# Kernel optimization log

Hardware: AMD Instinct MI355X
Metric: run time of the kernel (lower is better)

The kernel has to match this reference:

```python
import jax, jax.numpy as jnp
import numpy as np

D = 32       # d_model / hidden_size
H = 4        # n_heads
E = D // H   # head dim = 8
N = 2000     # nodes (hardcoded in FourierBlock weights / proj_class)
L = 96       # seq_len
MODES = (1, 4, 5)  # self.index hardcoded in FourierBlock
KAVG = 25    # moving_avg kernel (first of kernel list; layer uses res[0], trends[0])


def setup_inputs() -> dict:
    key = jax.random.key(0)
    ks = jax.random.split(key, 12)
    B = 8
    x = jax.random.normal(ks[0], (B, N, L, D), jnp.float32)
    lin = lambda k: jax.random.normal(k, (D, D), jnp.float32) * (1.0 / np.sqrt(D))
    scale = 1.0 / (D * D)  # FourierBlock: scale * torch.rand(...)
    W1 = jax.random.uniform(ks[5], (N, H, E, E, len(MODES)), jnp.float32) * scale
    W2 = jax.random.uniform(ks[6], (N, H, E, E, len(MODES)), jnp.float32) * scale
    return {
        "x": x,
        "Wq": lin(ks[1]), "bq": jnp.zeros((D,), jnp.float32),
        "Wk": lin(ks[2]), "bk": jnp.zeros((D,), jnp.float32),
        "Wv": lin(ks[3]), "bv": jnp.zeros((D,), jnp.float32),
        "Wo": lin(ks[4]), "bo": jnp.zeros((D,), jnp.float32),
        "W1": W1, "W2": W2,
    }


def _fourier_block(q, W1, W2):
    # q: [B, N, L, H, E] -> permute to [B, N, H, E, L] (torch: x = q.permute(0,1,3,4,2))
    B, Nn, Ll, Hh, Ee = q.shape
    xq = jnp.transpose(q, (0, 1, 3, 4, 2))
    x_ft = jnp.fft.rfft(xq, axis=-1)                 # [B, N, H, E, L//2+1] complex
    idx = jnp.array(MODES)
    xm = x_ft[..., idx]                              # [B, N, H, E, M]
    Wc = W1 + 1j * W2                                # complex per-node frequency weights
    out_m = jnp.einsum('bnhem,nheom->bnhom', xm, Wc.astype(jnp.complex64))
    F = Ll // 2 + 1
    out_ft = jnp.zeros((B, Nn, Hh, Ee, F), jnp.complex64).at[..., idx].set(out_m)
    y = jnp.fft.irfft(out_ft, n=Ll, axis=-1)         # [B, N, H, E, L]
    return jnp.transpose(y, (0, 1, 4, 2, 3))         # [B, N, L, H, E]


def _moving_avg(x, k):
    # replicate-pad the time axis by (k-1)//2 on each side, then mean over window k (stride 1)
    pad = (k - 1) // 2
    xp = jnp.pad(x, ((0, 0), (0, 0), (pad, pad), (0, 0)), mode='edge')
    cs = jnp.cumsum(xp, axis=2)
    cs = jnp.concatenate([jnp.zeros_like(cs[:, :, :1]), cs], axis=2)
    return (cs[:, :, k:] - cs[:, :, :-k]) / k        # [B, N, T, C]


def reference(x, Wq, bq, Wk, bk, Wv, bv, Wo, bo, W1, W2):
    B, Nn, Ll, Dm = x.shape
    # AutoCorrelationLayer projections
    q = (x @ Wq.T + bq).reshape(B, Nn, Ll, H, E)
    k = (x @ Wk.T + bk).reshape(B, Nn, Ll, H, E)   # faithful: computed, unused by FourierBlock
    v = (x @ Wv.T + bv).reshape(B, Nn, Ll, H, E)   # faithful: computed, unused by FourierBlock
    out = _fourier_block(q, W1, W2)                 # inner_correlation(q, k, v)
    out = out.reshape(B, Nn, Ll, Dm)
    new_x = out @ Wo.T + bo                         # out_projection
    # FFTDecompLayer: residual + series decomposition (eval mode, dropout=0)
    xr = x + new_x
    trend = _moving_avg(xr, KAVG)
    res = xr - trend
    return res
```

## Files before the change

kernel.cpp:

```cpp
#include <hip/hip_runtime.h>


#define N_NODES 2000

__global__ __launch_bounds__(256, 4)
void fused_fourier_decomp(const float* __restrict__ x,
                          const float* __restrict__ Wq,
                          const float* __restrict__ Wo,
                          const float* __restrict__ bo,
                          const float* __restrict__ W1,
                          const float* __restrict__ W2,
                          float* __restrict__ out)
{
  __shared__ __align__(16) float xT[32 * 97];
  __shared__ __align__(16) float basis[96 * 8];
  __shared__ __align__(16) float Wq_s[32 * 33];
  __shared__ __align__(16) float Wo_s[32 * 33];
  __shared__ __align__(16) float W1_s[768];
  __shared__ __align__(16) float W2_s[768];
  __shared__ __align__(16) float CS[32 * 8];
  __shared__ __align__(16) float X_s[32 * 8];
  __shared__ __align__(16) float O_s[32 * 8];
  __shared__ __align__(16) float Z_s[32 * 8];
  __shared__ float bo_s[32];
  float* const pp = xT;

  const int t = threadIdx.x;
  const int bid = blockIdx.x;
  const int n = bid % N_NODES;
  const size_t base = (size_t)bid * (96 * 32);

  const int d = t & 31;
  const int g = t >> 5;
  const int l0 = g * 12;

  float xv[12];
#pragma unroll
  for (int i = 0; i < 12; ++i)
    xv[i] = x[base + (size_t)(l0 + i) * 32 + d];

  for (int i = t; i < 1024; i += 256) {
    Wq_s[(i >> 5) * 33 + (i & 31)] = Wq[i];
    Wo_s[(i >> 5) * 33 + (i & 31)] = Wo[i];
  }
  {
    const float* W1p = W1 + n * 768;
    const float* W2p = W2 + n * 768;
    for (int i = t; i < 768; i += 256) {
      W1_s[i] = W1p[i];
      W2_s[i] = W2p[i];
    }
  }
  if (t < 32) bo_s[t] = bo[t];

  if (t < 96) {
    const int modes[3] = {1, 4, 5};
#pragma unroll
    for (int m = 0; m < 3; ++m) {
      int r = (modes[m] * t) % 96;
      float ang = (float)r * (6.28318530717958647692f / 96.0f);
      float sv, cv;
      sincosf(ang, &sv, &cv);
      basis[t * 8 + m] = cv;
      basis[t * 8 + 3 + m] = sv;
    }
    basis[t * 8 + 6] = 0.0f;
    basis[t * 8 + 7] = 0.0f;
  }
  __syncthreads();

  {
    float a0 = 0.f, a1 = 0.f, a2 = 0.f, a3 = 0.f, a4 = 0.f, a5 = 0.f;
#pragma unroll
    for (int i = 0; i < 12; ++i) {
      const int l = l0 + i;
      const float4 b0 = *(const float4*)&basis[l * 8];
      const float2 b1 = *(const float2*)&basis[l * 8 + 4];
      const float v = xv[i];
      a0 = fmaf(v, b0.x, a0);
      a1 = fmaf(v, b0.y, a1);
      a2 = fmaf(v, b0.z, a2);
      a3 = fmaf(v, b0.w, a3);
      a4 = fmaf(v, b1.x, a4);
      a5 = fmaf(v, b1.y, a5);
    }
    pp[g * 192 + 0 * 32 + d] = a0;
    pp[g * 192 + 1 * 32 + d] = a1;
    pp[g * 192 + 2 * 32 + d] = a2;
    pp[g * 192 + 3 * 32 + d] = a3;
    pp[g * 192 + 4 * 32 + d] = a4;
    pp[g * 192 + 5 * 32 + d] = a5;
  }
  __syncthreads();
  if (t < 192) {
    const int dd = t & 31, j = t >> 5;
    float s = 0.f;
#pragma unroll
    for (int gg = 0; gg < 8; ++gg) s += pp[gg * 192 + j * 32 + dd];
    CS[dd * 8 + j] = s;
  }
  __syncthreads();

  {
    float a0 = 0.f, a1 = 0.f, a2 = 0.f, a3 = 0.f, a4 = 0.f, a5 = 0.f;
#pragma unroll
    for (int i = 0; i < 4; ++i) {
      const int dd = g * 4 + i;
      const float w = Wq_s[d * 33 + dd];
      const float4 b0 = *(const float4*)&CS[dd * 8];
      const float2 b1 = *(const float2*)&CS[dd * 8 + 4];
      a0 = fmaf(w, b0.x, a0);
      a1 = fmaf(w, b0.y, a1);
      a2 = fmaf(w, b0.z, a2);
      a3 = fmaf(w, b0.w, a3);
      a4 = fmaf(w, b1.x, a4);
      a5 = fmaf(w, b1.y, a5);
    }
    pp[g * 192 + 0 * 32 + d] = a0;
    pp[g * 192 + 1 * 32 + d] = a1;
    pp[g * 192 + 2 * 32 + d] = a2;
    pp[g * 192 + 3 * 32 + d] = a3;
    pp[g * 192 + 4 * 32 + d] = a4;
    pp[g * 192 + 5 * 32 + d] = a5;
  }
  __syncthreads();
  if (t < 192) {
    const int c = t & 31, j = t >> 5;
    float s = 0.f;
#pragma unroll
    for (int gg = 0; gg < 8; ++gg) s += pp[gg * 192 + j * 32 + c];
    X_s[c * 8 + j] = (j < 3) ? s : -s;
  }
  __syncthreads();

  if (t < 96) {
    const int h = t / 24;
    const int r = t % 24;
    const int o = r / 3;
    const int m = r % 3;
    float re = 0.f, im = 0.f;
#pragma unroll
    for (int e = 0; e < 8; ++e) {
      const int c = h * 8 + e;
      const float xre = X_s[c * 8 + m];
      const float xim = X_s[c * 8 + 3 + m];
      const int wi = (c * 8 + o) * 3 + m;
      const float w1 = W1_s[wi], w2 = W2_s[wi];
      re = fmaf(xre, w1, re);
      re = fmaf(-xim, w2, re);
      im = fmaf(xre, w2, im);
      im = fmaf(xim, w1, im);
    }
    const int cp = h * 8 + o;
    O_s[cp * 8 + m] = re;
    O_s[cp * 8 + 3 + m] = im;
  }
  __syncthreads();

  {
    float a0 = 0.f, a1 = 0.f, a2 = 0.f, a3 = 0.f, a4 = 0.f, a5 = 0.f;
#pragma unroll
    for (int i = 0; i < 4; ++i) {
      const int c = g * 4 + i;
      const float w = Wo_s[d * 33 + c];
      const float4 b0 = *(const float4*)&O_s[c * 8];
      const float2 b1 = *(const float2*)&O_s[c * 8 + 4];
      a0 = fmaf(w, b0.x, a0);
      a1 = fmaf(w, b0.y, a1);
      a2 = fmaf(w, b0.z, a2);
      a3 = fmaf(w, b0.w, a3);
      a4 = fmaf(w, b1.x, a4);
      a5 = fmaf(w, b1.y, a5);
    }
    pp[g * 192 + 0 * 32 + d] = a0;
    pp[g * 192 + 1 * 32 + d] = a1;
    pp[g * 192 + 2 * 32 + d] = a2;
    pp[g * 192 + 3 * 32 + d] = a3;
    pp[g * 192 + 4 * 32 + d] = a4;
    pp[g * 192 + 5 * 32 + d] = a5;
  }
  __syncthreads();
  if (t < 192) {
    const int c = t & 31, j = t >> 5;
    float s = 0.f;
#pragma unroll
    for (int gg = 0; gg < 8; ++gg) s += pp[gg * 192 + j * 32 + c];
    Z_s[c * 8 + j] = s;
  }
  __syncthreads();

  float xr[12];
  {
    const float4 z0 = *(const float4*)&Z_s[d * 8];
    const float2 z1 = *(const float2*)&Z_s[d * 8 + 4];
    const float bov = bo_s[d];
#pragma unroll
    for (int i = 0; i < 12; ++i) {
      const int l = l0 + i;
      const float4 b0 = *(const float4*)&basis[l * 8];
      const float2 b1 = *(const float2*)&basis[l * 8 + 4];
      const float v = z0.x * b0.x + z0.y * b0.y + z0.z * b0.z
                    - z0.w * b0.w - z1.x * b1.x - z1.y * b1.y;
      const float r = fmaf(v, (1.0f / 48.0f), bov) + xv[i];
      xr[i] = r;
      xT[d * 97 + l] = r;
    }
  }
  __syncthreads();

  {
    const float* col = &xT[d * 97];
    float lowv[12];
    float S = 0.f;
#pragma unroll
    for (int j = 0; j < 12; ++j) {
      int idx = l0 - 12 + j;
      idx = idx < 0 ? 0 : idx;
      lowv[j] = col[idx];
      S += lowv[j];
    }
#pragma unroll
    for (int i = 0; i < 12; ++i) S += xr[i];
    {
      int idx = l0 + 12;
      idx = idx > 95 ? 95 : idx;
      S += col[idx];
    }
#pragma unroll
    for (int i = 0; i < 12; ++i) {
      const int l = l0 + i;
      const float res = xr[i] - S * (1.0f / 25.0f);
      out[base + (size_t)l * 32 + d] = res;
      int hi = l + 13;
      hi = hi > 95 ? 95 : hi;
      S += col[hi] - lowv[i];
    }
  }
}

extern "C" void kernel_launch(void* const* d_in, const int* in_sizes, int n_in,
                              void* d_out, int out_size, void* d_ws, size_t ws_size,
                              hipStream_t stream) {
  (void)n_in; (void)out_size; (void)d_ws; (void)ws_size;
  const float* x  = (const float*)d_in[0];
  const float* Wq = (const float*)d_in[1];
  const float* Wo = (const float*)d_in[7];
  const float* bo = (const float*)d_in[8];
  const float* W1 = (const float*)d_in[9];
  const float* W2 = (const float*)d_in[10];
  float* out = (float*)d_out;

  const int blocks = in_sizes[0] / (96 * 32);
  fused_fourier_decomp<<<blocks, 256, 0, stream>>>(x, Wq, Wo, bo, W1, W2, out);
}
```

Measured before the change: 386.2 us.

## Shrink shared memory, read weights from global, and raise occupancy target

Drops the per-block shared-memory staging of Wq, Wo, W1 and W2 and has the projection and mode-mixing stages read weights straight from global/L2. The Wq and Wo projections are restructured as a single 192-thread dot-product pass each, which removes one partial-sum stage and its barrier per projection. All scratch buffers are packed into one shared array with stride-9 padding, and the launch bounds request 8 blocks per CU. The aim is less shared memory and fewer barriers per block so more blocks fit per CU. The cost is redundant global weight reads and less thread-level parallelism in the projections.

```diff
diff --git a/kernel.cpp b/kernel.cpp
--- a/kernel.cpp
+++ b/kernel.cpp
@@ -3,7 +3,7 @@
 
 #define N_NODES 2000
 
-__global__ __launch_bounds__(256, 4)
+__global__ __launch_bounds__(256, 8)
 void fused_fourier_decomp(const float* __restrict__ x,
                           const float* __restrict__ Wq,
                           const float* __restrict__ Wo,
@@ -12,18 +12,15 @@
                           const float* __restrict__ W2,
                           float* __restrict__ out)
 {
-  __shared__ __align__(16) float xT[32 * 97];
-  __shared__ __align__(16) float basis[96 * 8];
-  __shared__ __align__(16) float Wq_s[32 * 33];
-  __shared__ __align__(16) float Wo_s[32 * 33];
-  __shared__ __align__(16) float W1_s[768];
-  __shared__ __align__(16) float W2_s[768];
-  __shared__ __align__(16) float CS[32 * 8];
-  __shared__ __align__(16) float X_s[32 * 8];
-  __shared__ __align__(16) float O_s[32 * 8];
-  __shared__ __align__(16) float Z_s[32 * 8];
-  __shared__ float bo_s[32];
-  float* const pp = xT;
+  __shared__ __align__(16) float smem[5056];
+  float* const basis = smem;
+  float* const CS    = smem + 768;
+  float* const Xs    = smem + 1056;
+  float* const Os    = smem + 1344;
+  float* const Zs    = smem + 1632;
+  float* const bos   = smem + 1920;
+  float* const xT    = smem + 1952;
+  float* const pp    = smem + 1952;
 
   const int t = threadIdx.x;
   const int bid = blockIdx.x;
@@ -34,24 +31,12 @@
   const int g = t >> 5;
   const int l0 = g * 12;
 
+  const float* xp = x + base + (size_t)l0 * 32 + d;
   float xv[12];
 #pragma unroll
-  for (int i = 0; i < 12; ++i)
-    xv[i] = x[base + (size_t)(l0 + i) * 32 + d];
-
-  for (int i = t; i < 1024; i += 256) {
-    Wq_s[(i >> 5) * 33 + (i & 31)] = Wq[i];
-    Wo_s[(i >> 5) * 33 + (i & 31)] = Wo[i];
-  }
-  {
-    const float* W1p = W1 + n * 768;
-    const float* W2p = W2 + n * 768;
-    for (int i = t; i < 768; i += 256) {
-      W1_s[i] = W1p[i];
-      W2_s[i] = W2p[i];
-    }
-  }
-  if (t < 32) bo_s[t] = bo[t];
+  for (int i = 0; i < 12; ++i) xv[i] = xp[i * 32];
+
+  if (t < 32) bos[t] = bo[t];
 
   if (t < 96) {
     const int modes[3] = {1, 4, 5};
@@ -97,110 +82,82 @@
     float s = 0.f;
 #pragma unroll
     for (int gg = 0; gg < 8; ++gg) s += pp[gg * 192 + j * 32 + dd];
-    CS[dd * 8 + j] = s;
-  }
-  __syncthreads();
-
-  {
-    float a0 = 0.f, a1 = 0.f, a2 = 0.f, a3 = 0.f, a4 = 0.f, a5 = 0.f;
-#pragma unroll
-    for (int i = 0; i < 4; ++i) {
-      const int dd = g * 4 + i;
-      const float w = Wq_s[d * 33 + dd];
-      const float4 b0 = *(const float4*)&CS[dd * 8];
-      const float2 b1 = *(const float2*)&CS[dd * 8 + 4];
-      a0 = fmaf(w, b0.x, a0);
-      a1 = fmaf(w, b0.y, a1);
-      a2 = fmaf(w, b0.z, a2);
-      a3 = fmaf(w, b0.w, a3);
-      a4 = fmaf(w, b1.x, a4);
-      a5 = fmaf(w, b1.y, a5);
-    }
-    pp[g * 192 + 0 * 32 + d] = a0;
-    pp[g * 192 + 1 * 32 + d] = a1;
-    pp[g * 192 + 2 * 32 + d] = a2;
-    pp[g * 192 + 3 * 32 + d] = a3;
-    pp[g * 192 + 4 * 32 + d] = a4;
-    pp[g * 192 + 5 * 32 + d] = a5;
-  }
-  __syncthreads();
+    CS[dd * 9 + j] = s;
+  }
+  __syncthreads();
+
   if (t < 192) {
     const int c = t & 31, j = t >> 5;
+    const float4* wq4 = (const float4*)(Wq + c * 32);
     float s = 0.f;
 #pragma unroll
-    for (int gg = 0; gg < 8; ++gg) s += pp[gg * 192 + j * 32 + c];
-    X_s[c * 8 + j] = (j < 3) ? s : -s;
+    for (int q = 0; q < 8; ++q) {
+      const float4 w = wq4[q];
+      const int dd = q * 4;
+      s = fmaf(w.x, CS[(dd + 0) * 9 + j], s);
+      s = fmaf(w.y, CS[(dd + 1) * 9 + j], s);
+      s = fmaf(w.z, CS[(dd + 2) * 9 + j], s);
+      s = fmaf(w.w, CS[(dd + 3) * 9 + j], s);
+    }
+    Xs[c * 9 + j] = (j < 3) ? s : -s;
   }
   __syncthreads();
 
   if (t < 96) {
     const int h = t / 24;
-    const int r = t % 24;
+    const int r = t - h * 24;
     const int o = r / 3;
-    const int m = r % 3;
+    const int m = r - o * 3;
+    const float* W1p = W1 + n * 768;
+    const float* W2p = W2 + n * 768;
     float re = 0.f, im = 0.f;
 #pragma unroll
     for (int e = 0; e < 8; ++e) {
       const int c = h * 8 + e;
-      const float xre = X_s[c * 8 + m];
-      const float xim = X_s[c * 8 + 3 + m];
+      const float xre = Xs[c * 9 + m];
+      const float xim = Xs[c * 9 + 3 + m];
       const int wi = (c * 8 + o) * 3 + m;
-      const float w1 = W1_s[wi], w2 = W2_s[wi];
+      const float w1 = W1p[wi], w2 = W2p[wi];
       re = fmaf(xre, w1, re);
       re = fmaf(-xim, w2, re);
       im = fmaf(xre, w2, im);
       im = fmaf(xim, w1, im);
     }
     const int cp = h * 8 + o;
-    O_s[cp * 8 + m] = re;
-    O_s[cp * 8 + 3 + m] = im;
-  }
-  __syncthreads();
-
-  {
-    float a0 = 0.f, a1 = 0.f, a2 = 0.f, a3 = 0.f, a4 = 0.f, a5 = 0.f;
-#pragma unroll
-    for (int i = 0; i < 4; ++i) {
-      const int c = g * 4 + i;
-      const float w = Wo_s[d * 33 + c];
-      const float4 b0 = *(const float4*)&O_s[c * 8];
-      const float2 b1 = *(const float2*)&O_s[c * 8 + 4];
-      a0 = fmaf(w, b0.x, a0);
-      a1 = fmaf(w, b0.y, a1);
-      a2 = fmaf(w, b0.z, a2);
-      a3 = fmaf(w, b0.w, a3);
-      a4 = fmaf(w, b1.x, a4);
-      a5 = fmaf(w, b1.y, a5);
-    }
-    pp[g * 192 + 0 * 32 + d] = a0;
-    pp[g * 192 + 1 * 32 + d] = a1;
-    pp[g * 192 + 2 * 32 + d] = a2;
-    pp[g * 192 + 3 * 32 + d] = a3;
-    pp[g * 192 + 4 * 32 + d] = a4;
-    pp[g * 192 + 5 * 32 + d] = a5;
-  }
-  __syncthreads();
+    Os[cp * 9 + m] = re;
+    Os[cp * 9 + 3 + m] = im;
+  }
+  __syncthreads();
+
   if (t < 192) {
     const int c = t & 31, j = t >> 5;
+    const float4* wo4 = (const float4*)(Wo + c * 32);
     float s = 0.f;
 #pragma unroll
-    for (int gg = 0; gg < 8; ++gg) s += pp[gg * 192 + j * 32 + c];
-    Z_s[c * 8 + j] = s;
+    for (int q = 0; q < 8; ++q) {
+      const float4 w = wo4[q];
+      const int cc = q * 4;
+      s = fmaf(w.x, Os[(cc + 0) * 9 + j], s);
+      s = fmaf(w.y, Os[(cc + 1) * 9 + j], s);
+      s = fmaf(w.z, Os[(cc + 2) * 9 + j], s);
+      s = fmaf(w.w, Os[(cc + 3) * 9 + j], s);
+    }
+    Zs[c * 9 + j] = s;
   }
   __syncthreads();
 
   float xr[12];
   {
-    const float4 z0 = *(const float4*)&Z_s[d * 8];
-    const float2 z1 = *(const float2*)&Z_s[d * 8 + 4];
-    const float bov = bo_s[d];
+    const float zre0 = Zs[d * 9 + 0], zre1 = Zs[d * 9 + 1], zre2 = Zs[d * 9 + 2];
+    const float zim0 = Zs[d * 9 + 3], zim1 = Zs[d * 9 + 4], zim2 = Zs[d * 9 + 5];
+    const float bov = bos[d];
 #pragma unroll
     for (int i = 0; i < 12; ++i) {
       const int l = l0 + i;
       const float4 b0 = *(const float4*)&basis[l * 8];
       const float2 b1 = *(const float2*)&basis[l * 8 + 4];
-      const float v = z0.x * b0.x + z0.y * b0.y + z0.z * b0.z
-                    - z0.w * b0.w - z1.x * b1.x - z1.y * b1.y;
+      const float v = zre0 * b0.x + zre1 * b0.y + zre2 * b0.z
+                    - zim0 * b0.w - zim1 * b1.x - zim2 * b1.y;
       const float r = fmaf(v, (1.0f / 48.0f), bov) + xv[i];
       xr[i] = r;
       xT[d * 97 + l] = r;
@@ -210,6 +167,7 @@
 
   {
     const float* col = &xT[d * 97];
+    float* op = out + base + (size_t)l0 * 32 + d;
     float lowv[12];
     float S = 0.f;
 #pragma unroll
@@ -229,8 +187,7 @@
 #pragma unroll
     for (int i = 0; i < 12; ++i) {
       const int l = l0 + i;
-      const float res = xr[i] - S * (1.0f / 25.0f);
-      out[base + (size_t)l * 32 + d] = res;
+      op[i * 32] = xr[i] - S * (1.0f / 25.0f);
       int hi = l + 13;
       hi = hi > 95 ? 95 : hi;
       S += col[hi] - lowv[i];
```

New measurement: 398.5 us. 3.2% more time.
